# Kernel optimization log

Measured on AMD Instinct MI355X. Metric: run time of the kernel, lower is better.

## Reference

```python
import jax, jax.numpy as jnp
import numpy as np

ALPHA = 0.2  # LeakyReLU negative slope
NEG_INF = -9e15


def setup_inputs() -> dict:
    key = jax.random.key(0)
    k1, k2, k3, k4, k5 = jax.random.split(key, 5)
    B, N, D = 4, 4096, 256
    feat = jax.random.normal(k1, (B, N, D), dtype=jnp.float32)
    adj = jax.random.randint(k2, (B, N, N), 0, 2, dtype=jnp.int32)
    W = jax.random.normal(k3, (D, D), dtype=jnp.float32) * (1.414 / np.sqrt(D))
    a_1 = jax.random.normal(k4, (D, 1), dtype=jnp.float32) * 0.1
    a_2 = jax.random.normal(k5, (D, 1), dtype=jnp.float32) * 0.1
    return {"feat": feat, "adj": adj, "W": W, "a_1": a_1, "a_2": a_2}


def reference(feat, adj, W, a_1, a_2):
    # h: [B, N, D]
    h = jnp.matmul(feat, W)
    Ax = jnp.matmul(h, a_1)  # [B, N, 1]
    Ay = jnp.matmul(h, a_2)  # [B, N, 1]
    # logits[b, i, j] = Ax[b, j] + Ay[b, i]
    logits = jnp.swapaxes(Ax, 1, 2) + Ay  # [B, N, N]
    e = jax.nn.leaky_relu(logits, negative_slope=ALPHA)
    e = jnp.where(adj > 0, e, jnp.float32(NEG_INF))
    attention = jax.nn.softmax(e, axis=-1)  # dropout p=0.0 -> identity
    h_prime = jnp.matmul(attention, feat)  # [B, N, in_features]
    h_out = jnp.matmul(h_prime, W)  # [B, N, out_features]
    return jax.nn.elu(h_out)
```

## Files before the change

### kernel.cpp

```cpp
#include <hip/hip_runtime.h>

typedef __attribute__((ext_vector_type(8))) short short8;
typedef __attribute__((ext_vector_type(4))) float f32x4;
typedef __attribute__((ext_vector_type(4))) int i32x4;
typedef __attribute__((ext_vector_type(2))) unsigned u32x2;

#define LOG2E 1.44269504f
#define FT_STRIDE 4128
#define FT_BATCH (256 * FT_STRIDE)

__device__ __forceinline__ short f2bf(float f) {
  unsigned u = __builtin_bit_cast(unsigned, f);
  u += 0x7fffu + ((u >> 16) & 1u);
  return (short)(u >> 16);
}

__global__ void gat_wvec(const float* __restrict__ W, const float* __restrict__ a1,
                         const float* __restrict__ a2, float* __restrict__ w1,
                         float* __restrict__ w2) {
  __shared__ float a1f[256], a2f[256];
  const int tid = threadIdx.x;
  a1f[tid] = a1[tid];
  a2f[tid] = a2[tid];
  __syncthreads();
  float s1 = 0.f, s2 = 0.f;
  const float4* wr = (const float4*)(W + (size_t)tid * 256);
  for (int d0 = 0; d0 < 64; ++d0) {
    float4 v = wr[d0];
    s1 += v.x * a1f[d0 * 4] + v.y * a1f[d0 * 4 + 1] + v.z * a1f[d0 * 4 + 2] + v.w * a1f[d0 * 4 + 3];
    s2 += v.x * a2f[d0 * 4] + v.y * a2f[d0 * 4 + 1] + v.z * a2f[d0 * 4 + 2] + v.w * a2f[d0 * 4 + 3];
  }
  w1[tid] = s1;
  w2[tid] = s2;
}

__global__ void convT(const float* __restrict__ src, short* __restrict__ dst,
                      int R, int C, int dstStride, size_t dstBatch) {
  __shared__ short T[64][72];
  const int tid = threadIdx.x;
  const int bc = blockIdx.x, br = blockIdx.y, bb = blockIdx.z;
  const float* s = src + (size_t)bb * R * C;
  short* d = dst + (size_t)bb * dstBatch;
  const int rr = tid >> 2, cc = (tid & 3) << 4;
  const float4* sp = (const float4*)(s + (size_t)(br * 64 + rr) * C + bc * 64 + cc);
  alignas(16) short v[16];
#pragma unroll
  for (int g = 0; g < 4; ++g) {
    float4 x = sp[g];
    v[g * 4 + 0] = f2bf(x.x);
    v[g * 4 + 1] = f2bf(x.y);
    v[g * 4 + 2] = f2bf(x.z);
    v[g * 4 + 3] = f2bf(x.w);
  }
  *(short8*)&T[rr][cc] = *(short8*)&v[0];
  *(short8*)&T[rr][cc + 8] = *(short8*)&v[8];
  __syncthreads();
#pragma unroll
  for (int j = 0; j < 16; ++j) v[j] = T[cc + j][rr];
  short8* dp = (short8*)(d + (size_t)(bc * 64 + rr) * dstStride + br * 64 + cc);
  dp[0] = *(short8*)&v[0];
  dp[1] = *(short8*)&v[8];
}

__global__ void gat_axay(const float* __restrict__ feat, const float* __restrict__ w1,
                         const float* __restrict__ w2, float* __restrict__ AxL,
                         float* __restrict__ AyL) {
  const int lane = threadIdx.x & 63;
  const int row = blockIdx.x * 4 + (threadIdx.x >> 6);
  float4 fv = *(const float4*)(feat + (size_t)row * 256 + lane * 4);
  const float4 w1v = *(const float4*)(w1 + lane * 4);
  const float4 w2v = *(const float4*)(w2 + lane * 4);
  float s1 = fv.x * w1v.x + fv.y * w1v.y + fv.z * w1v.z + fv.w * w1v.w;
  float s2 = fv.x * w2v.x + fv.y * w2v.y + fv.z * w2v.z + fv.w * w2v.w;
#pragma unroll
  for (int off = 32; off >= 1; off >>= 1) {
    s1 += __shfl_xor(s1, off);
    s2 += __shfl_xor(s2, off);
  }
  if (lane == 0) { AxL[row] = s1 * LOG2E; AyL[row] = s2 * LOG2E; }
}

__global__ void gat_max(const float* __restrict__ AxL, float* __restrict__ MbL) {
  __shared__ float red[256];
  const int b = blockIdx.x, tid = threadIdx.x;
  float m = -3.4e38f;
  for (int i = tid; i < 4096; i += 256) m = fmaxf(m, AxL[b * 4096 + i]);
  red[tid] = m;
  __syncthreads();
  for (int s = 128; s > 0; s >>= 1) {
    if (tid < s) red[tid] = fmaxf(red[tid], red[tid + s]);
    __syncthreads();
  }
  if (tid == 0) MbL[b] = red[0];
}

__global__ __launch_bounds__(512, 4) void gat_attn(
    const short* __restrict__ featT,
    const int* __restrict__ adj,
    const float* __restrict__ AxL, const float* __restrict__ AyL,
    const float* __restrict__ MbL,
    const short* __restrict__ WT,
    float* __restrict__ out)
{
  __shared__ short smem[37376];

  const int tid = threadIdx.x;
  const int blk = blockIdx.x;
  const int x = blk & 7;
  const int b = x >> 1;
  const int it = ((blk >> 3) << 1) | (x & 1);
  const int i0 = it << 5;

  const int pi = tid >> 4;
  const int pj = tid & 15;
  const float ayL = AyL[b * 4096 + i0 + pi];
  const float sL = ayL + MbL[b];
  const float mrL = fmaxf(sL, 0.2f * sL);
  const float aL = ayL - mrL;
  const float dd = -0.8f * mrL;

  const int sn = tid >> 3;
  const int so = tid & 7;
  const int sph = ((so ^ (sn & 7)) << 3);

  const int lane = tid & 63;
  const int w = tid >> 6;
  const int rowg = (w & 1) << 4;
  const int colg = (w >> 1) << 6;
  const int l15 = lane & 15;
  const int q = lane >> 4;
  const int swz = l15 & 7;
  const int bu0 = (q ^ swz) << 3;
  const int bu1 = ((q + 4) ^ swz) << 3;

  f32x4 acc[4], lac;
  lac = (f32x4){0.f, 0.f, 0.f, 0.f};
#pragma unroll
  for (int j = 0; j < 4; ++j) acc[j] = (f32x4){0.f, 0.f, 0.f, 0.f};

  short8 ones;
#pragma unroll
  for (int j = 0; j < 8; ++j) ones[j] = (short)0x3F80;

  const i32x4* adjp = (const i32x4*)(adj + ((size_t)(b * 4096 + i0 + pi)) * 4096) + pj;
  const float4* axp = (const float4*)(AxL + b * 4096) + pj;
  const short* ftb = featT + (size_t)b * FT_BATCH + (size_t)sn * FT_STRIDE + so * 8;

  i32x4 adv;
  float4 axv;
  short8 bv[4];
  adv = __builtin_nontemporal_load(adjp);
  axv = axp[0];
#pragma unroll
  for (int k = 0; k < 4; ++k) bv[k] = *(const short8*)(ftb + (size_t)k * 64 * FT_STRIDE);

  for (int jc = 0; jc < 64; ++jc) {
    const int pb = jc & 1;
    {
      const float* af = (const float*)&axv;
      unsigned pr[4];
#pragma unroll
      for (int u = 0; u < 4; ++u) {
        float v = af[u] + aL;
        float uu = fmaxf(v, fmaf(0.2f, v, dd));
        unsigned ub = adv[u] > 0 ? __builtin_bit_cast(unsigned, uu) : 0xFF800000u;
        float p = __builtin_amdgcn_exp2f(__builtin_bit_cast(float, ub));
        pr[u] = __builtin_bit_cast(unsigned, p) + 0x8000u;
      }
      u32x2 pw;
      pw[0] = __builtin_amdgcn_perm(pr[1], pr[0], 0x07060302u);
      pw[1] = __builtin_amdgcn_perm(pr[3], pr[2], 0x07060302u);
      *(u32x2*)(smem + 32768 + pb * 2304 + pi * 72 + pj * 4) = pw;
    }
    {
      short* bs = smem + pb * 16384;
#pragma unroll
      for (int k = 0; k < 4; ++k)
        *(short8*)(bs + (sn + 64 * k) * 64 + sph) = bv[k];
    }
    __syncthreads();

    if (jc < 63) {
      adv = __builtin_nontemporal_load(adjp + (jc + 1) * 16);
      axv = axp[(jc + 1) * 16];
#pragma unroll
      for (int k = 0; k < 4; ++k)
        bv[k] = *(const short8*)(ftb + (size_t)k * 64 * FT_STRIDE + (jc + 1) * 64);
    }

    const short* pbuf = smem + 32768 + pb * 2304;
    const short* bsr = smem + pb * 16384;
#pragma unroll
    for (int h = 0; h < 2; ++h) {
      const int k0 = h * 32;
      const int bu = h ? bu1 : bu0;
      short8 a = *(const short8*)(pbuf + (rowg + l15) * 72 + k0 + q * 8);
      lac = __builtin_amdgcn_mfma_f32_16x16x32_bf16(a, ones, lac, 0, 0, 0);
#pragma unroll
      for (int ct = 0; ct < 4; ++ct) {
        short8 bf = *(const short8*)(bsr + (colg + ct * 16 + l15) * 64 + bu);
        acc[ct] = __builtin_amdgcn_mfma_f32_16x16x32_bf16(a, bf, acc[ct], 0, 0, 0);
      }
    }
  }

  float linv[4];
#pragma unroll
  for (int reg = 0; reg < 4; ++reg) {
    float l = lac[reg];
    linv[reg] = l > 0.f ? 1.f / l : 0.f;
  }

  __syncthreads();
  short* hbuf = smem;
#pragma unroll
  for (int reg = 0; reg < 4; ++reg) {
    const int lr = rowg + q * 4 + reg;
#pragma unroll
    for (int ct = 0; ct < 4; ++ct)
      hbuf[lr * 264 + colg + ct * 16 + l15] = f2bf(acc[ct][reg] * linv[reg]);
  }
  __syncthreads();

  f32x4 ac2[4];
#pragma unroll
  for (int j = 0; j < 4; ++j) ac2[j] = (f32x4){0.f, 0.f, 0.f, 0.f};

#pragma unroll 2
  for (int k0 = 0; k0 < 256; k0 += 32) {
    short8 a = *(const short8*)&hbuf[(rowg + l15) * 264 + k0 + q * 8];
#pragma unroll
    for (int ct = 0; ct < 4; ++ct) {
      short8 bf = *(const short8*)(WT + (size_t)(colg + ct * 16 + l15) * 256 + k0 + q * 8);
      ac2[ct] = __builtin_amdgcn_mfma_f32_16x16x32_bf16(a, bf, ac2[ct], 0, 0, 0);
    }
  }

#pragma unroll
  for (int reg = 0; reg < 4; ++reg) {
    const int row = i0 + rowg + q * 4 + reg;
    float* orow = out + ((size_t)(b * 4096 + row)) * 256 + colg + l15;
#pragma unroll
    for (int ct = 0; ct < 4; ++ct) {
      float v = ac2[ct][reg];
      float o = v > 0.f ? v : (__builtin_amdgcn_exp2f(v * LOG2E) - 1.f);
      __builtin_nontemporal_store(o, orow + ct * 16);
    }
  }
}

extern "C" void kernel_launch(void* const* d_in, const int* in_sizes, int n_in,
                              void* d_out, int out_size, void* d_ws, size_t ws_size,
                              hipStream_t stream) {
  (void)in_sizes; (void)n_in; (void)out_size; (void)ws_size;
  const float* feat = (const float*)d_in[0];
  const int* adj = (const int*)d_in[1];
  const float* W = (const float*)d_in[2];
  const float* a1 = (const float*)d_in[3];
  const float* a2 = (const float*)d_in[4];
  float* out = (float*)d_out;

  char* ws = (char*)d_ws;
  short* featT   = (short*)ws;
  short* WT      = (short*)(ws + 8454144);
  float* AxL     = (float*)(ws + 8585216);
  float* AyL     = (float*)(ws + 8650752);
  float* MbL     = (float*)(ws + 8716288);
  float* w1      = (float*)(ws + 8717312);
  float* w2      = (float*)(ws + 8718336);

  hipLaunchKernelGGL(gat_wvec, dim3(1), dim3(256), 0, stream, W, a1, a2, w1, w2);
  hipLaunchKernelGGL(convT, dim3(4, 4, 1), dim3(256), 0, stream, W, WT, 256, 256, 256, (size_t)65536);
  hipLaunchKernelGGL(convT, dim3(4, 64, 4), dim3(256), 0, stream, feat, featT, 4096, 256, FT_STRIDE, (size_t)FT_BATCH);
  hipLaunchKernelGGL(gat_axay, dim3(4096), dim3(256), 0, stream, feat, w1, w2, AxL, AyL);
  hipLaunchKernelGGL(gat_max, dim3(4), dim3(256), 0, stream, AxL, MbL);
  hipLaunchKernelGGL(gat_attn, dim3(512), dim3(512), 0, stream, featT, adj, AxL, AyL, MbL, WT, out);
}
```

Baseline: 466.6 us.

## Pre-pack feat and W into MFMA fragment layout, read B operand directly from global

Replaces the transpose-to-bf16 kernel with a packing kernel that writes feat and W in the exact per-lane MFMA B-fragment order. The attention kernel then loads B fragments straight from global/L2 instead of staging them through double-buffered shared memory, which shrinks LDS use and removes the LDS store traffic. The trade-off is that every wave now issues global loads for the B tiles inside the inner loop without register prefetch, so latency may be exposed, and the four row-group waves re-read the same data from cache.

```diff
diff --git a/kernel.cpp b/kernel.cpp
--- a/kernel.cpp
+++ b/kernel.cpp
@@ -6,8 +6,6 @@
 typedef __attribute__((ext_vector_type(2))) unsigned u32x2;
 
 #define LOG2E 1.44269504f
-#define FT_STRIDE 4128
-#define FT_BATCH (256 * FT_STRIDE)
 
 __device__ __forceinline__ short f2bf(float f) {
   unsigned u = __builtin_bit_cast(unsigned, f);
@@ -34,32 +32,19 @@
   w2[tid] = s2;
 }
 
-__global__ void convT(const float* __restrict__ src, short* __restrict__ dst,
-                      int R, int C, int dstStride, size_t dstBatch) {
-  __shared__ short T[64][72];
+__global__ void packB(const float* __restrict__ src, short* __restrict__ dst, int F) {
   const int tid = threadIdx.x;
-  const int bc = blockIdx.x, br = blockIdx.y, bb = blockIdx.z;
-  const float* s = src + (size_t)bb * R * C;
-  short* d = dst + (size_t)bb * dstBatch;
-  const int rr = tid >> 2, cc = (tid & 3) << 4;
-  const float4* sp = (const float4*)(s + (size_t)(br * 64 + rr) * C + bc * 64 + cc);
-  alignas(16) short v[16];
-#pragma unroll
-  for (int g = 0; g < 4; ++g) {
-    float4 x = sp[g];
-    v[g * 4 + 0] = f2bf(x.x);
-    v[g * 4 + 1] = f2bf(x.y);
-    v[g * 4 + 2] = f2bf(x.z);
-    v[g * 4 + 3] = f2bf(x.w);
-  }
-  *(short8*)&T[rr][cc] = *(short8*)&v[0];
-  *(short8*)&T[rr][cc + 8] = *(short8*)&v[8];
-  __syncthreads();
-#pragma unroll
-  for (int j = 0; j < 16; ++j) v[j] = T[cc + j][rr];
-  short8* dp = (short8*)(d + (size_t)(bc * 64 + rr) * dstStride + br * 64 + cc);
-  dp[0] = *(short8*)&v[0];
-  dp[1] = *(short8*)&v[8];
+  const int f = blockIdx.x, b = blockIdx.y;
+  const int g = tid >> 4, l15 = tid & 15;
+  const float* s = src + ((size_t)b * F * 32 + f * 32) * 256 + g * 16 + l15;
+  short* d = dst + (((size_t)(b * F + f) * 16 + g) * 64) * 8;
+#pragma unroll
+  for (int q = 0; q < 4; ++q) {
+    short8 v;
+#pragma unroll
+    for (int j8 = 0; j8 < 8; ++j8) v[j8] = f2bf(s[(q * 8 + j8) * 256]);
+    *(short8*)(d + (q * 16 + l15) * 8) = v;
+  }
 }
 
 __global__ void gat_axay(const float* __restrict__ feat, const float* __restrict__ w1,
@@ -95,14 +80,14 @@
 }
 
 __global__ __launch_bounds__(512, 4) void gat_attn(
-    const short* __restrict__ featT,
+    const short* __restrict__ featB,
     const int* __restrict__ adj,
     const float* __restrict__ AxL, const float* __restrict__ AyL,
     const float* __restrict__ MbL,
-    const short* __restrict__ WT,
+    const short* __restrict__ WB,
     float* __restrict__ out)
 {
-  __shared__ short smem[37376];
+  __shared__ short smem[8448];
 
   const int tid = threadIdx.x;
   const int blk = blockIdx.x;
@@ -119,19 +104,12 @@
   const float aL = ayL - mrL;
   const float dd = -0.8f * mrL;
 
-  const int sn = tid >> 3;
-  const int so = tid & 7;
-  const int sph = ((so ^ (sn & 7)) << 3);
-
   const int lane = tid & 63;
   const int w = tid >> 6;
   const int rowg = (w & 1) << 4;
-  const int colg = (w >> 1) << 6;
+  const int cgrp = (w >> 1) << 2;
   const int l15 = lane & 15;
   const int q = lane >> 4;
-  const int swz = l15 & 7;
-  const int bu0 = (q ^ swz) << 3;
-  const int bu1 = ((q + 4) ^ swz) << 3;
 
   f32x4 acc[4], lac;
   lac = (f32x4){0.f, 0.f, 0.f, 0.f};
@@ -144,18 +122,13 @@
 
   const i32x4* adjp = (const i32x4*)(adj + ((size_t)(b * 4096 + i0 + pi)) * 4096) + pj;
   const float4* axp = (const float4*)(AxL + b * 4096) + pj;
-  const short* ftb = featT + (size_t)b * FT_BATCH + (size_t)sn * FT_STRIDE + so * 8;
-
-  i32x4 adv;
-  float4 axv;
-  short8 bv[4];
-  adv = __builtin_nontemporal_load(adjp);
-  axv = axp[0];
-#pragma unroll
-  for (int k = 0; k < 4; ++k) bv[k] = *(const short8*)(ftb + (size_t)k * 64 * FT_STRIDE);
+  const short* fbb = featB + (size_t)b * 128 * 16 * 64 * 8 + lane * 8;
+
+  i32x4 adv = __builtin_nontemporal_load(adjp);
+  float4 axv = axp[0];
 
   for (int jc = 0; jc < 64; ++jc) {
-    const int pb = jc & 1;
+    const int pb = (jc & 1) * 2304;
     {
       const float* af = (const float*)&axv;
       unsigned pr[4];
@@ -170,35 +143,23 @@
       u32x2 pw;
       pw[0] = __builtin_amdgcn_perm(pr[1], pr[0], 0x07060302u);
       pw[1] = __builtin_amdgcn_perm(pr[3], pr[2], 0x07060302u);
-      *(u32x2*)(smem + 32768 + pb * 2304 + pi * 72 + pj * 4) = pw;
-    }
-    {
-      short* bs = smem + pb * 16384;
-#pragma unroll
-      for (int k = 0; k < 4; ++k)
-        *(short8*)(bs + (sn + 64 * k) * 64 + sph) = bv[k];
+      *(u32x2*)(smem + pb + pi * 72 + pj * 4) = pw;
     }
     __syncthreads();
 
     if (jc < 63) {
       adv = __builtin_nontemporal_load(adjp + (jc + 1) * 16);
       axv = axp[(jc + 1) * 16];
-#pragma unroll
-      for (int k = 0; k < 4; ++k)
-        bv[k] = *(const short8*)(ftb + (size_t)k * 64 * FT_STRIDE + (jc + 1) * 64);
-    }
-
-    const short* pbuf = smem + 32768 + pb * 2304;
-    const short* bsr = smem + pb * 16384;
+    }
+
 #pragma unroll
     for (int h = 0; h < 2; ++h) {
-      const int k0 = h * 32;
-      const int bu = h ? bu1 : bu0;
-      short8 a = *(const short8*)(pbuf + (rowg + l15) * 72 + k0 + q * 8);
+      const short* fb = fbb + (((size_t)(jc * 2 + h) * 16 + cgrp) << 9);
+      short8 a = *(const short8*)(smem + pb + (rowg + l15) * 72 + h * 32 + q * 8);
       lac = __builtin_amdgcn_mfma_f32_16x16x32_bf16(a, ones, lac, 0, 0, 0);
 #pragma unroll
       for (int ct = 0; ct < 4; ++ct) {
-        short8 bf = *(const short8*)(bsr + (colg + ct * 16 + l15) * 64 + bu);
+        short8 bf = *(const short8*)(fb + (ct << 9));
         acc[ct] = __builtin_amdgcn_mfma_f32_16x16x32_bf16(a, bf, acc[ct], 0, 0, 0);
       }
     }
@@ -218,7 +179,7 @@
     const int lr = rowg + q * 4 + reg;
 #pragma unroll
     for (int ct = 0; ct < 4; ++ct)
-      hbuf[lr * 264 + colg + ct * 16 + l15] = f2bf(acc[ct][reg] * linv[reg]);
+      hbuf[lr * 264 + cgrp * 16 + ct * 16 + l15] = f2bf(acc[ct][reg] * linv[reg]);
   }
   __syncthreads();
 
@@ -226,12 +187,14 @@
 #pragma unroll
   for (int j = 0; j < 4; ++j) ac2[j] = (f32x4){0.f, 0.f, 0.f, 0.f};
 
-#pragma unroll 2
-  for (int k0 = 0; k0 < 256; k0 += 32) {
-    short8 a = *(const short8*)&hbuf[(rowg + l15) * 264 + k0 + q * 8];
+  const short* wbb = WB + lane * 8;
+#pragma unroll
+  for (int f = 0; f < 8; ++f) {
+    short8 a = *(const short8*)&hbuf[(rowg + l15) * 264 + f * 32 + q * 8];
+    const short* wb = wbb + (((size_t)f * 16 + cgrp) << 9);
 #pragma unroll
     for (int ct = 0; ct < 4; ++ct) {
-      short8 bf = *(const short8*)(WT + (size_t)(colg + ct * 16 + l15) * 256 + k0 + q * 8);
+      short8 bf = *(const short8*)(wb + (ct << 9));
       ac2[ct] = __builtin_amdgcn_mfma_f32_16x16x32_bf16(a, bf, ac2[ct], 0, 0, 0);
     }
   }
@@ -239,7 +202,7 @@
 #pragma unroll
   for (int reg = 0; reg < 4; ++reg) {
     const int row = i0 + rowg + q * 4 + reg;
-    float* orow = out + ((size_t)(b * 4096 + row)) * 256 + colg + l15;
+    float* orow = out + ((size_t)(b * 4096 + row)) * 256 + cgrp * 16 + l15;
 #pragma unroll
     for (int ct = 0; ct < 4; ++ct) {
       float v = ac2[ct][reg];
@@ -261,18 +224,18 @@
   float* out = (float*)d_out;
 
   char* ws = (char*)d_ws;
-  short* featT   = (short*)ws;
-  short* WT      = (short*)(ws + 8454144);
-  float* AxL     = (float*)(ws + 8585216);
-  float* AyL     = (float*)(ws + 8650752);
-  float* MbL     = (float*)(ws + 8716288);
-  float* w1      = (float*)(ws + 8717312);
-  float* w2      = (float*)(ws + 8718336);
+  short* featB   = (short*)ws;
+  short* WB      = (short*)(ws + 8388608);
+  float* AxL     = (float*)(ws + 8519680);
+  float* AyL     = (float*)(ws + 8585216);
+  float* MbL     = (float*)(ws + 8650752);
+  float* w1      = (float*)(ws + 8651776);
+  float* w2      = (float*)(ws + 8652800);
 
   hipLaunchKernelGGL(gat_wvec, dim3(1), dim3(256), 0, stream, W, a1, a2, w1, w2);
-  hipLaunchKernelGGL(convT, dim3(4, 4, 1), dim3(256), 0, stream, W, WT, 256, 256, 256, (size_t)65536);
-  hipLaunchKernelGGL(convT, dim3(4, 64, 4), dim3(256), 0, stream, feat, featT, 4096, 256, FT_STRIDE, (size_t)FT_BATCH);
+  hipLaunchKernelGGL(packB, dim3(8, 1), dim3(256), 0, stream, W, WB, 8);
+  hipLaunchKernelGGL(packB, dim3(128, 4), dim3(256), 0, stream, feat, featB, 128);
   hipLaunchKernelGGL(gat_axay, dim3(4096), dim3(256), 0, stream, feat, w1, w2, AxL, AyL);
   hipLaunchKernelGGL(gat_max, dim3(4), dim3(256), 0, stream, AxL, MbL);
-  hipLaunchKernelGGL(gat_attn, dim3(512), dim3(512), 0, stream, featT, adj, AxL, AyL, MbL, WT, out);
-}
+  hipLaunchKernelGGL(gat_attn, dim3(512), dim3(512), 0, stream, featB, adj, AxL, AyL, MbL, WB, out);
+}
```

Result: slower. 476.7 us (+2.2%).
